# Kernel optimization log

Hardware: AMD Instinct MI355X
Metric: run time of the kernel (lower is better)

Reference implementation:

```python
import jax, jax.numpy as jnp
import numpy as np

CH = 128
GROUPS = 8
EPS = 1e-5


def setup_inputs() -> dict:
    key = jax.random.key(0)
    ks = jax.random.split(key, 12)
    b, c, h, w = 16, CH, 64, 64
    x = jax.random.normal(ks[0], (b, c, h, w), dtype=jnp.float32)
    s = 1.0 / np.sqrt(c)
    return {
        "x": x,
        "gn_w": jnp.ones((c,), jnp.float32),
        "gn_b": jnp.zeros((c,), jnp.float32),
        "wq": jax.random.normal(ks[1], (c, c), jnp.float32) * s,
        "bq": jax.random.normal(ks[2], (c,), jnp.float32) * 0.01,
        "wk": jax.random.normal(ks[3], (c, c), jnp.float32) * s,
        "bk": jax.random.normal(ks[4], (c,), jnp.float32) * 0.01,
        "wv": jax.random.normal(ks[5], (c, c), jnp.float32) * s,
        "bv": jax.random.normal(ks[6], (c,), jnp.float32) * 0.01,
        "wf": jax.random.normal(ks[7], (c, c), jnp.float32) * s,
        "bf": jax.random.normal(ks[8], (c,), jnp.float32) * 0.01,
    }


def _group_norm(x, gamma, beta):
    b, c, h, w = x.shape
    xg = x.reshape(b, GROUPS, -1)  # [b, g, (c/g)*h*w]
    mean = xg.mean(axis=-1, keepdims=True)
    var = xg.var(axis=-1, keepdims=True)
    xn = ((xg - mean) * jax.lax.rsqrt(var + EPS)).reshape(b, c, h, w)
    return xn * gamma[None, :, None, None] + beta[None, :, None, None]


def reference(x, gn_w, gn_b, wq, bq, wk, bk, wv, bv, wf, bf):
    b, c, h, w = x.shape
    x_gn = _group_norm(x, gn_w, gn_b)
    xf = x_gn.reshape(b, c, h * w)  # [b, c, n]
    # 1x1 convs == per-position channel matmuls
    q = jnp.einsum('oc,bcn->bon', wq, xf) + bq[None, :, None]
    k = jnp.einsum('oc,bcn->bon', wk, xf) + bk[None, :, None]
    v = jnp.einsum('oc,bcn->bon', wv, xf) + bv[None, :, None]
    scale = c ** (-0.5)
    attn = jnp.einsum('bci,bcj->bij', q, k) * scale  # [b, n, n]
    attn = jax.nn.softmax(attn, axis=-1)
    # out[b,c,i] = sum_j v[b,c,j] * attn[b,i,j]
    o = jnp.einsum('bcj,bij->bci', v, attn)
    of = jnp.einsum('oc,bcn->bon', wf, o) + bf[None, :, None]
    return of.reshape(b, c, h, w) + x
```

## Files before the change

### kernel.cpp

```cpp
#include <hip/hip_runtime.h>

#define NB   16
#define NC   128
#define NPOS 4096

typedef short bf16x8 __attribute__((ext_vector_type(8)));
typedef float f32x4  __attribute__((ext_vector_type(4)));
typedef float f32x16 __attribute__((ext_vector_type(16)));
typedef unsigned int u32x4 __attribute__((ext_vector_type(4)));

#define SCF 0.12751743075095855f

static __device__ __forceinline__ unsigned short f2bf(float f) {
    unsigned int u = __builtin_bit_cast(unsigned int, f);
    u += 0x7FFFu + ((u >> 16) & 1u);
    return (unsigned short)(u >> 16);
}

static __device__ __forceinline__ unsigned int pkbf(float hi, float lo) {
    return __builtin_amdgcn_perm(__builtin_bit_cast(unsigned int, hi),
                                 __builtin_bit_cast(unsigned int, lo), 0x07060302u);
}

static __device__ __forceinline__ float vmax16(const f32x16 v) {
    float a = fmaxf(fmaxf(v[0], v[1]), fmaxf(v[2], v[3]));
    float b = fmaxf(fmaxf(v[4], v[5]), fmaxf(v[6], v[7]));
    float c = fmaxf(fmaxf(v[8], v[9]), fmaxf(v[10], v[11]));
    float d = fmaxf(fmaxf(v[12], v[13]), fmaxf(v[14], v[15]));
    return fmaxf(fmaxf(a, b), fmaxf(c, d));
}

static __device__ __forceinline__ float vsum16(const float* p) {
    float a = (p[0] + p[1]) + (p[2] + p[3]);
    float b = (p[4] + p[5]) + (p[6] + p[7]);
    float c = (p[8] + p[9]) + (p[10] + p[11]);
    float d = (p[12] + p[13]) + (p[14] + p[15]);
    return (a + b) + (c + d);
}

static __device__ __forceinline__ void mk_bfrag_pair(const float* pp, bf16x8* dst, int h) {
    #pragma unroll
    for (int c2 = 0; c2 < 2; ++c2) {
        int rb = c2 * 8;
        unsigned int A0 = pkbf(pp[rb + 1], pp[rb + 0]);
        unsigned int A1 = pkbf(pp[rb + 3], pp[rb + 2]);
        unsigned int B0 = pkbf(pp[rb + 5], pp[rb + 4]);
        unsigned int B1 = pkbf(pp[rb + 7], pp[rb + 6]);
        unsigned int s0 = h ? A0 : B0, s1 = h ? A1 : B1;
        unsigned int r0 = __shfl_xor(s0, 32), r1 = __shfl_xor(s1, 32);
        u32x4 f;
        f[0] = h ? r0 : A0; f[1] = h ? r1 : A1;
        f[2] = h ? B0 : r0; f[3] = h ? B1 : r1;
        dst[c2] = __builtin_bit_cast(bf16x8, f);
    }
}

static __device__ __forceinline__ void stage_tile(unsigned short* lds, const unsigned short* g,
                                                  int t, int w) {
    #pragma unroll
    for (int c = 0; c < 4; ++c) {
        __builtin_amdgcn_global_load_lds(
            (const __attribute__((address_space(1))) unsigned int*)(g + c * 2048 + t * 8),
            (__attribute__((address_space(3))) unsigned int*)(lds + c * 2048 + w * 512),
            16, 0, 0);
    }
}

__global__ void wconv_kernel(const float* __restrict__ wq, const float* __restrict__ wk,
                             const float* __restrict__ wv, const float* __restrict__ wf,
                             unsigned short* __restrict__ oq, unsigned short* __restrict__ ok,
                             unsigned short* __restrict__ ov, unsigned short* __restrict__ of) {
    int i = blockIdx.x * 256 + threadIdx.x;
    oq[i] = f2bf(wq[i]); ok[i] = f2bf(wk[i]); ov[i] = f2bf(wv[i]); of[i] = f2bf(wf[i]);
}

__global__ void gnstat_kernel(const float* __restrict__ x, float* __restrict__ mean,
                              float* __restrict__ rstd) {
    int bg = blockIdx.x;
    const float* p = x + (size_t)bg * 65536;
    int t = threadIdx.x;
    float s = 0.f, q = 0.f;
    for (int it = 0; it < 64; ++it) {
        f32x4 v = *(const f32x4*)(p + it * 1024 + t * 4);
        s += v[0] + v[1] + v[2] + v[3];
        q += v[0] * v[0] + v[1] * v[1] + v[2] * v[2] + v[3] * v[3];
    }
    for (int m = 1; m < 64; m <<= 1) { s += __shfl_xor(s, m); q += __shfl_xor(q, m); }
    __shared__ float ls[4], lq[4];
    int w = t >> 6;
    if ((t & 63) == 0) { ls[w] = s; lq[w] = q; }
    __syncthreads();
    if (t == 0) {
        s = ls[0] + ls[1] + ls[2] + ls[3];
        q = lq[0] + lq[1] + lq[2] + lq[3];
        float mu  = s * (1.0f / 65536.0f);
        float var = q * (1.0f / 65536.0f) - mu * mu;
        mean[bg] = mu;
        rstd[bg] = rsqrtf(var + 1e-5f);
    }
}

__global__ __launch_bounds__(256) void qkv_kernel(
    const float* __restrict__ x, const float* __restrict__ gnw, const float* __restrict__ gnb,
    const float* __restrict__ mean, const float* __restrict__ rstd,
    const unsigned short* __restrict__ wqb, const unsigned short* __restrict__ wkb,
    const unsigned short* __restrict__ wvb,
    const float* __restrict__ bq, const float* __restrict__ bk, const float* __restrict__ bv,
    unsigned short* __restrict__ qT, unsigned short* __restrict__ Kf, unsigned short* __restrict__ Vf) {
    __shared__ __attribute__((aligned(16))) unsigned short xn[64 * 136];
    __shared__ __attribute__((aligned(16))) unsigned short bnc[64 * 128];
    const int b = blockIdx.y, i0 = blockIdx.x * 64, jt = blockIdx.x;
    const int t = threadIdx.x;
    {
        int iL = (t & 15) * 4;
        int cb = (t >> 4) * 2;
        for (int cg = 0; cg < 4; ++cg) {
            int c = cg * 32 + cb;
            int g = c >> 4;
            float mu = mean[b * 8 + g], rs = rstd[b * 8 + g];
            float ga0 = gnw[c] * rs,     be0 = gnb[c]     - mu * ga0;
            float ga1 = gnw[c + 1] * rs, be1 = gnb[c + 1] - mu * ga1;
            const float* p0 = x + ((size_t)(b * NC + c)) * NPOS + i0 + iL;
            f32x4 v0 = *(const f32x4*)p0;
            f32x4 v1 = *(const f32x4*)(p0 + NPOS);
            for (int e = 0; e < 4; ++e) {
                unsigned int u = (unsigned)f2bf(v0[e] * ga0 + be0) |
                                 ((unsigned)f2bf(v1[e] * ga1 + be1) << 16);
                *(unsigned int*)&xn[(iL + e) * 136 + c] = u;
            }
        }
    }
    __syncthreads();

    const int lane = t & 63, w = t >> 6, quad = lane >> 4, li = lane & 15;

    bf16x8 ax[4];
    for (int kc = 0; kc < 4; ++kc)
        ax[kc] = *(const bf16x8*)&xn[(w * 16 + li) * 136 + kc * 32 + quad * 8];

    for (int wt = 0; wt < 2; ++wt) {
        const unsigned short* W = wt ? wkb : wqb;
        const float* bias = wt ? bk : bq;
        const float osc = wt ? 1.0f : SCF;
        for (int nt = 0; nt < 8; ++nt) {
            f32x4 d = {0.f, 0.f, 0.f, 0.f};
            for (int kc = 0; kc < 4; ++kc) {
                bf16x8 bw = *(const bf16x8*)&W[(nt * 16 + li) * 128 + kc * 32 + quad * 8];
                d = __builtin_amdgcn_mfma_f32_16x16x32_bf16(ax[kc], bw, d, 0, 0, 0);
            }
            float bb = bias[nt * 16 + li];
            int o = nt * 16 + li;
            for (int rr = 0; rr < 4; ++rr) {
                int i = w * 16 + quad * 4 + rr;
                bnc[i * 128 + (((o >> 3) ^ (i & 7)) << 3) + (o & 7)] = f2bf((d[rr] + bb) * osc);
            }
        }
        __syncthreads();
        if (wt == 0) {
            unsigned short* dst = qT + ((size_t)b * NPOS + i0) * NC + t * 32;
            int i = t >> 2;
            for (int s = 0; s < 4; ++s) {
                int cc = (t & 3) * 4 + s;
                *(bf16x8*)(dst + s * 8) = *(const bf16x8*)&bnc[i * 128 + ((cc ^ (i & 7)) << 3)];
            }
        } else {
            unsigned short* dst = Kf + ((size_t)(b * 64 + jt)) * 8192 + t * 32;
            int F = t >> 4, jtile = F >> 3, kc = F & 7;
            for (int s = 0; s < 4; ++s) {
                int L = (t * 4 + s) & 63;
                int i = jtile * 32 + (L & 31);
                int cc = kc * 2 + (L >> 5);
                *(bf16x8*)(dst + s * 8) = *(const bf16x8*)&bnc[i * 128 + ((cc ^ (i & 7)) << 3)];
            }
        }
        __syncthreads();
    }

    bf16x8 av[2][4];
    for (int mt = 0; mt < 2; ++mt)
        for (int kc = 0; kc < 4; ++kc)
            av[mt][kc] = *(const bf16x8*)&wvb[((w * 2 + mt) * 16 + li) * 128 + kc * 32 + quad * 8];
    for (int nt = 0; nt < 4; ++nt) {
        bf16x8 bx[4];
        for (int kc = 0; kc < 4; ++kc)
            bx[kc] = *(const bf16x8*)&xn[(nt * 16 + li) * 136 + kc * 32 + quad * 8];
        for (int mt = 0; mt < 2; ++mt) {
            f32x4 d = {0.f, 0.f, 0.f, 0.f};
            for (int kc = 0; kc < 4; ++kc)
                d = __builtin_amdgcn_mfma_f32_16x16x32_bf16(av[mt][kc], bx[kc], d, 0, 0, 0);
            int o0 = (w * 2 + mt) * 16 + quad * 4;
            int j = nt * 16 + li;
            for (int rr = 0; rr < 4; ++rr) {
                int c = o0 + rr;
                bnc[c * 64 + (((j >> 3) ^ (c & 7)) << 3) + (j & 7)] = f2bf(d[rr] + bv[c]);
            }
        }
    }
    __syncthreads();
    {
        unsigned short* dst = Vf + ((size_t)(b * 64 + jt)) * 8192 + t * 32;
        int F = t >> 4, ct = F >> 2, kc2 = F & 3;
        for (int s = 0; s < 4; ++s) {
            int L = (t * 4 + s) & 63;
            int c = ct * 32 + (L & 31);
            int jc = kc2 * 2 + (L >> 5);
            *(bf16x8*)(dst + s * 8) = *(const bf16x8*)&bnc[c * 64 + ((jc ^ (c & 7)) << 3)];
        }
    }
}

__global__ __launch_bounds__(256, 2) void flash_kernel(
    const unsigned short* __restrict__ qT, const unsigned short* __restrict__ Kf,
    const unsigned short* __restrict__ Vf, const unsigned short* __restrict__ wfb,
    const float* __restrict__ bf_, const float* __restrict__ x, float* __restrict__ out) {
    __shared__ __attribute__((aligned(16))) unsigned short KV[2][2][8192];
    const int idx = blockIdx.x;
    const int b = (idx & 7) * 2 + ((idx >> 3) & 1);
    const int rg = idx >> 4;
    const int t = threadIdx.x, lane = t & 63, w = t >> 6;
    const int il = lane & 31, h = lane >> 5;
    const int iw = (rg * 4 + w) * 32;

    const unsigned short* Kb = Kf + ((size_t)b * 64) * 8192;
    const unsigned short* Vb = Vf + ((size_t)b * 64) * 8192;

    stage_tile(&KV[0][0][0], Kb, t, w);
    stage_tile(&KV[0][1][0], Vb, t, w);

    bf16x8 qb[8];
    #pragma unroll
    for (int kc = 0; kc < 8; ++kc)
        qb[kc] = *(const bf16x8*)&qT[((size_t)b * NPOS + iw + il) * NC + kc * 16 + h * 8];

    float mr = -1e30f, lr = 0.f;
    f32x16 acc[4];
    #pragma unroll
    for (int ct = 0; ct < 4; ++ct)
        #pragma unroll
        for (int q = 0; q < 16; ++q) acc[ct][q] = 0.f;

    __syncthreads();

    for (int jt = 0; jt < 64; ++jt) {
        const int cur = jt & 1;
        const unsigned short* kl = &KV[cur][0][0] + lane * 8;
        const unsigned short* vl = &KV[cur][1][0] + lane * 8;
        if (jt < 63) {
            stage_tile(&KV[cur ^ 1][0][0], Kb + (size_t)(jt + 1) * 8192, t, w);
            stage_tile(&KV[cur ^ 1][1][0], Vb + (size_t)(jt + 1) * 8192, t, w);
        }

        f32x16 st[2];
        #pragma unroll
        for (int u = 0; u < 2; ++u)
            #pragma unroll
            for (int q = 0; q < 16; ++q) st[u][q] = 0.f;
        __builtin_amdgcn_s_setprio(1);
        #pragma unroll
        for (int kc = 0; kc < 8; ++kc) {
            bf16x8 k0 = *(const bf16x8*)(kl + kc * 512);
            bf16x8 k1 = *(const bf16x8*)(kl + (8 + kc) * 512);
            st[0] = __builtin_amdgcn_mfma_f32_32x32x16_bf16(k0, qb[kc], st[0], 0, 0, 0);
            st[1] = __builtin_amdgcn_mfma_f32_32x32x16_bf16(k1, qb[kc], st[1], 0, 0, 0);
        }
        __builtin_amdgcn_s_setprio(0);

        float mx = fmaxf(vmax16(st[0]), vmax16(st[1]));
        mx = fmaxf(mx, __shfl_xor(mx, 32));
        if (__any(mx > mr)) {
            float mn = fmaxf(mr, mx);
            float alpha = __builtin_amdgcn_exp2f(mr - mn);
            mr = mn;
            lr *= alpha;
            #pragma unroll
            for (int ct = 0; ct < 4; ++ct)
                #pragma unroll
                for (int q = 0; q < 16; ++q) acc[ct][q] *= alpha;
        }
        float mc = mr - 0.0028150156f;
        #pragma unroll
        for (int q = 0; q < 16; ++q) {
            st[0][q] = __builtin_amdgcn_exp2f(st[0][q] - mc);
            st[1][q] = __builtin_amdgcn_exp2f(st[1][q] - mc);
        }
        float rs = vsum16((const float*)&st[0]) + vsum16((const float*)&st[1]);
        rs += __shfl_xor(rs, 32);
        lr += rs;

        bf16x8 pfrag[4];
        mk_bfrag_pair((const float*)&st[0], &pfrag[0], h);
        mk_bfrag_pair((const float*)&st[1], &pfrag[2], h);

        __builtin_amdgcn_s_setprio(1);
        #pragma unroll
        for (int ct = 0; ct < 4; ++ct)
            #pragma unroll
            for (int kc2 = 0; kc2 < 4; ++kc2) {
                bf16x8 vfm = *(const bf16x8*)(vl + (ct * 4 + kc2) * 512);
                acc[ct] = __builtin_amdgcn_mfma_f32_32x32x16_bf16(vfm, pfrag[kc2],
                                                                  acc[ct], 0, 0, 0);
            }
        __builtin_amdgcn_s_setprio(0);

        __syncthreads();
    }

    bf16x8 obf[8];
    {
        float inv = __builtin_amdgcn_rcpf(lr) * 1.001953125f;
        #pragma unroll
        for (int ct = 0; ct < 4; ++ct) {
            float pp[16];
            #pragma unroll
            for (int q = 0; q < 16; ++q) pp[q] = acc[ct][q] * inv;
            mk_bfrag_pair(pp, &obf[ct * 2], h);
        }
    }

    #pragma unroll
    for (int ot = 0; ot < 4; ++ot) {
        bf16x8 wfA[8];
        #pragma unroll
        for (int kc = 0; kc < 8; ++kc)
            wfA[kc] = *(const bf16x8*)&wfb[(ot * 32 + il) * 128 + kc * 16 + h * 8];
        f32x16 d;
        #pragma unroll
        for (int q = 0; q < 16; ++q) d[q] = 0.f;
        #pragma unroll
        for (int kc = 0; kc < 8; ++kc)
            d = __builtin_amdgcn_mfma_f32_32x32x16_bf16(wfA[kc], obf[kc], d, 0, 0, 0);
        const int gi = iw + il;
        #pragma unroll
        for (int q = 0; q < 16; ++q) {
            int o = ot * 32 + (q & 3) + 8 * (q >> 2) + 4 * h;
            size_t a = ((size_t)(b * NC + o)) * NPOS + gi;
            out[a] = d[q] + bf_[o] + x[a];
        }
    }
}

extern "C" void kernel_launch(void* const* d_in, const int* in_sizes, int n_in,
                              void* d_out, int out_size, void* d_ws, size_t ws_size,
                              hipStream_t stream) {
    const float* x   = (const float*)d_in[0];
    const float* gnw = (const float*)d_in[1];
    const float* gnb = (const float*)d_in[2];
    const float* wq  = (const float*)d_in[3];
    const float* bq  = (const float*)d_in[4];
    const float* wk  = (const float*)d_in[5];
    const float* bk  = (const float*)d_in[6];
    const float* wv  = (const float*)d_in[7];
    const float* bv  = (const float*)d_in[8];
    const float* wf  = (const float*)d_in[9];
    const float* bf_ = (const float*)d_in[10];
    float* out = (float*)d_out;

    char* ws = (char*)d_ws;
    float* mean = (float*)(ws + 0);
    float* rstd = (float*)(ws + 512);
    unsigned short* wqb = (unsigned short*)(ws + 1024);
    unsigned short* wkb = wqb + 16384;
    unsigned short* wvb = wkb + 16384;
    unsigned short* wfb = wvb + 16384;
    unsigned short* qT  = (unsigned short*)(ws + 132096);
    unsigned short* Kf  = qT + (size_t)NB * NPOS * NC;
    unsigned short* Vf  = Kf + (size_t)NB * NPOS * NC;

    wconv_kernel<<<64, 256, 0, stream>>>(wq, wk, wv, wf, wqb, wkb, wvb, wfb);
    gnstat_kernel<<<128, 256, 0, stream>>>(x, mean, rstd);
    dim3 g(64, 16);
    qkv_kernel<<<g, 256, 0, stream>>>(x, gnw, gnb, mean, rstd, wqb, wkb, wvb, bq, bk, bv, qT, Kf, Vf);
    flash_kernel<<<512, 256, 0, stream>>>(qT, Kf, Vf, wfb, bf_, x, out);
}
```

Baseline: 315.3 us.

## Process two 32-query groups per wave to reuse K/V fragments

Each wave now handles 64 query rows as two 32-row groups that share every K and V fragment read from shared memory, with separate softmax state and accumulators per group. Grid size is halved to 256 blocks and launch bounds drop to one block per SM to make room for the doubled register footprint. The aim is to halve LDS reads and K/V staging per unit of work and give the MFMA units more independent work. In exchange, 256 blocks may underfill the device's compute units, and the lower occupancy reduces latency hiding.

```diff
diff --git a/kernel.cpp b/kernel.cpp
--- a/kernel.cpp
+++ b/kernel.cpp
@@ -209,7 +209,7 @@
     }
 }
 
-__global__ __launch_bounds__(256, 2) void flash_kernel(
+__global__ __launch_bounds__(256, 1) void flash_kernel(
     const unsigned short* __restrict__ qT, const unsigned short* __restrict__ Kf,
     const unsigned short* __restrict__ Vf, const unsigned short* __restrict__ wfb,
     const float* __restrict__ bf_, const float* __restrict__ x, float* __restrict__ out) {
@@ -219,7 +219,7 @@
     const int rg = idx >> 4;
     const int t = threadIdx.x, lane = t & 63, w = t >> 6;
     const int il = lane & 31, h = lane >> 5;
-    const int iw = (rg * 4 + w) * 32;
+    const int iw = (rg * 4 + w) * 64;
 
     const unsigned short* Kb = Kf + ((size_t)b * 64) * 8192;
     const unsigned short* Vb = Vf + ((size_t)b * 64) * 8192;
@@ -227,17 +227,21 @@
     stage_tile(&KV[0][0][0], Kb, t, w);
     stage_tile(&KV[0][1][0], Vb, t, w);
 
-    bf16x8 qb[8];
-    #pragma unroll
-    for (int kc = 0; kc < 8; ++kc)
-        qb[kc] = *(const bf16x8*)&qT[((size_t)b * NPOS + iw + il) * NC + kc * 16 + h * 8];
-
-    float mr = -1e30f, lr = 0.f;
-    f32x16 acc[4];
-    #pragma unroll
-    for (int ct = 0; ct < 4; ++ct)
-        #pragma unroll
-        for (int q = 0; q < 16; ++q) acc[ct][q] = 0.f;
+    bf16x8 qb[2][8];
+    #pragma unroll
+    for (int ig = 0; ig < 2; ++ig)
+        #pragma unroll
+        for (int kc = 0; kc < 8; ++kc)
+            qb[ig][kc] = *(const bf16x8*)&qT[((size_t)b * NPOS + iw + ig * 32 + il) * NC + kc * 16 + h * 8];
+
+    float mr[2] = {-1e30f, -1e30f}, lr[2] = {0.f, 0.f};
+    f32x16 acc[2][4];
+    #pragma unroll
+    for (int ig = 0; ig < 2; ++ig)
+        #pragma unroll
+        for (int ct = 0; ct < 4; ++ct)
+            #pragma unroll
+            for (int q = 0; q < 16; ++q) acc[ig][ct][q] = 0.f;
 
     __syncthreads();
 
@@ -250,9 +254,9 @@
             stage_tile(&KV[cur ^ 1][1][0], Vb + (size_t)(jt + 1) * 8192, t, w);
         }
 
-        f32x16 st[2];
-        #pragma unroll
-        for (int u = 0; u < 2; ++u)
+        f32x16 st[4];
+        #pragma unroll
+        for (int u = 0; u < 4; ++u)
             #pragma unroll
             for (int q = 0; q < 16; ++q) st[u][q] = 0.f;
         __builtin_amdgcn_s_setprio(1);
@@ -260,36 +264,40 @@
         for (int kc = 0; kc < 8; ++kc) {
             bf16x8 k0 = *(const bf16x8*)(kl + kc * 512);
             bf16x8 k1 = *(const bf16x8*)(kl + (8 + kc) * 512);
-            st[0] = __builtin_amdgcn_mfma_f32_32x32x16_bf16(k0, qb[kc], st[0], 0, 0, 0);
-            st[1] = __builtin_amdgcn_mfma_f32_32x32x16_bf16(k1, qb[kc], st[1], 0, 0, 0);
+            st[0] = __builtin_amdgcn_mfma_f32_32x32x16_bf16(k0, qb[0][kc], st[0], 0, 0, 0);
+            st[2] = __builtin_amdgcn_mfma_f32_32x32x16_bf16(k0, qb[1][kc], st[2], 0, 0, 0);
+            st[1] = __builtin_amdgcn_mfma_f32_32x32x16_bf16(k1, qb[0][kc], st[1], 0, 0, 0);
+            st[3] = __builtin_amdgcn_mfma_f32_32x32x16_bf16(k1, qb[1][kc], st[3], 0, 0, 0);
         }
         __builtin_amdgcn_s_setprio(0);
 
-        float mx = fmaxf(vmax16(st[0]), vmax16(st[1]));
-        mx = fmaxf(mx, __shfl_xor(mx, 32));
-        if (__any(mx > mr)) {
-            float mn = fmaxf(mr, mx);
-            float alpha = __builtin_amdgcn_exp2f(mr - mn);
-            mr = mn;
-            lr *= alpha;
-            #pragma unroll
-            for (int ct = 0; ct < 4; ++ct)
+        bf16x8 pfrag[2][4];
+        #pragma unroll
+        for (int ig = 0; ig < 2; ++ig) {
+            float mx = fmaxf(vmax16(st[ig * 2]), vmax16(st[ig * 2 + 1]));
+            mx = fmaxf(mx, __shfl_xor(mx, 32));
+            if (__any(mx > mr[ig])) {
+                float mn = fmaxf(mr[ig], mx);
+                float alpha = __builtin_amdgcn_exp2f(mr[ig] - mn);
+                mr[ig] = mn;
+                lr[ig] *= alpha;
                 #pragma unroll
-                for (int q = 0; q < 16; ++q) acc[ct][q] *= alpha;
-        }
-        float mc = mr - 0.0028150156f;
-        #pragma unroll
-        for (int q = 0; q < 16; ++q) {
-            st[0][q] = __builtin_amdgcn_exp2f(st[0][q] - mc);
-            st[1][q] = __builtin_amdgcn_exp2f(st[1][q] - mc);
-        }
-        float rs = vsum16((const float*)&st[0]) + vsum16((const float*)&st[1]);
-        rs += __shfl_xor(rs, 32);
-        lr += rs;
-
-        bf16x8 pfrag[4];
-        mk_bfrag_pair((const float*)&st[0], &pfrag[0], h);
-        mk_bfrag_pair((const float*)&st[1], &pfrag[2], h);
+                for (int ct = 0; ct < 4; ++ct)
+                    #pragma unroll
+                    for (int q = 0; q < 16; ++q) acc[ig][ct][q] *= alpha;
+            }
+            float mc = mr[ig] - 0.0028150156f;
+            #pragma unroll
+            for (int q = 0; q < 16; ++q) {
+                st[ig * 2][q]     = __builtin_amdgcn_exp2f(st[ig * 2][q] - mc);
+                st[ig * 2 + 1][q] = __builtin_amdgcn_exp2f(st[ig * 2 + 1][q] - mc);
+            }
+            float rs = vsum16((const float*)&st[ig * 2]) + vsum16((const float*)&st[ig * 2 + 1]);
+            rs += __shfl_xor(rs, 32);
+            lr[ig] += rs;
+            mk_bfrag_pair((const float*)&st[ig * 2],     &pfrag[ig][0], h);
+            mk_bfrag_pair((const float*)&st[ig * 2 + 1], &pfrag[ig][2], h);
+        }
 
         __builtin_amdgcn_s_setprio(1);
         #pragma unroll
@@ -297,23 +305,26 @@
             #pragma unroll
             for (int kc2 = 0; kc2 < 4; ++kc2) {
                 bf16x8 vfm = *(const bf16x8*)(vl + (ct * 4 + kc2) * 512);
-                acc[ct] = __builtin_amdgcn_mfma_f32_32x32x16_bf16(vfm, pfrag[kc2],
-                                                                  acc[ct], 0, 0, 0);
+                acc[0][ct] = __builtin_amdgcn_mfma_f32_32x32x16_bf16(vfm, pfrag[0][kc2],
+                                                                     acc[0][ct], 0, 0, 0);
+                acc[1][ct] = __builtin_amdgcn_mfma_f32_32x32x16_bf16(vfm, pfrag[1][kc2],
+                                                                     acc[1][ct], 0, 0, 0);
             }
         __builtin_amdgcn_s_setprio(0);
 
         __syncthreads();
     }
 
-    bf16x8 obf[8];
-    {
-        float inv = __builtin_amdgcn_rcpf(lr) * 1.001953125f;
+    bf16x8 obf[2][8];
+    #pragma unroll
+    for (int ig = 0; ig < 2; ++ig) {
+        float inv = __builtin_amdgcn_rcpf(lr[ig]) * 1.001953125f;
         #pragma unroll
         for (int ct = 0; ct < 4; ++ct) {
             float pp[16];
             #pragma unroll
-            for (int q = 0; q < 16; ++q) pp[q] = acc[ct][q] * inv;
-            mk_bfrag_pair(pp, &obf[ct * 2], h);
+            for (int q = 0; q < 16; ++q) pp[q] = acc[ig][ct][q] * inv;
+            mk_bfrag_pair(pp, &obf[ig][ct * 2], h);
         }
     }
 
@@ -323,18 +334,21 @@
         #pragma unroll
         for (int kc = 0; kc < 8; ++kc)
             wfA[kc] = *(const bf16x8*)&wfb[(ot * 32 + il) * 128 + kc * 16 + h * 8];
-        f32x16 d;
-        #pragma unroll
-        for (int q = 0; q < 16; ++q) d[q] = 0.f;
-        #pragma unroll
-        for (int kc = 0; kc < 8; ++kc)
-            d = __builtin_amdgcn_mfma_f32_32x32x16_bf16(wfA[kc], obf[kc], d, 0, 0, 0);
-        const int gi = iw + il;
-        #pragma unroll
-        for (int q = 0; q < 16; ++q) {
-            int o = ot * 32 + (q & 3) + 8 * (q >> 2) + 4 * h;
-            size_t a = ((size_t)(b * NC + o)) * NPOS + gi;
-            out[a] = d[q] + bf_[o] + x[a];
+        #pragma unroll
+        for (int ig = 0; ig < 2; ++ig) {
+            f32x16 d;
+            #pragma unroll
+            for (int q = 0; q < 16; ++q) d[q] = 0.f;
+            #pragma unroll
+            for (int kc = 0; kc < 8; ++kc)
+                d = __builtin_amdgcn_mfma_f32_32x32x16_bf16(wfA[kc], obf[ig][kc], d, 0, 0, 0);
+            const int gi = iw + ig * 32 + il;
+            #pragma unroll
+            for (int q = 0; q < 16; ++q) {
+                int o = ot * 32 + (q & 3) + 8 * (q >> 2) + 4 * h;
+                size_t a = ((size_t)(b * NC + o)) * NPOS + gi;
+                out[a] = d[q] + bf_[o] + x[a];
+            }
         }
     }
 }
@@ -370,5 +384,5 @@
     gnstat_kernel<<<128, 256, 0, stream>>>(x, mean, rstd);
     dim3 g(64, 16);
     qkv_kernel<<<g, 256, 0, stream>>>(x, gnw, gnb, mean, rstd, wqb, wkb, wvb, bq, bk, bv, qT, Kf, Vf);
-    flash_kernel<<<512, 256, 0, stream>>>(qT, Kf, Vf, wfb, bf_, x, out);
-}
+    flash_kernel<<<256, 256, 0, stream>>>(qT, Kf, Vf, wfb, bf_, x, out);
+}
```

After: 366.1 us. 1.16x slower.
